# Optimization experiments

Hardware: AMD Instinct MI355X
Metric: run time of the kernel (lower is better)

Reference implementation:

```python
import jax, jax.numpy as jnp
import numpy as np

WINDOW = 47
PAD = WINDOW // 2


def _box_sum(x):
    """Separable 47x47 box-filter SUM with zero padding (NHWC).

    Mathematically identical to a full 2-D window sum but O(W) per pixel
    instead of O(W^2).
    """
    x = jax.lax.reduce_window(
        x, 0.0, jax.lax.add,
        window_dimensions=(1, WINDOW, 1, 1), window_strides=(1, 1, 1, 1),
        padding=[(0, 0), (PAD, PAD), (0, 0), (0, 0)])
    x = jax.lax.reduce_window(
        x, 0.0, jax.lax.add,
        window_dimensions=(1, 1, WINDOW, 1), window_strides=(1, 1, 1, 1),
        padding=[(0, 0), (0, 0), (PAD, PAD), (0, 0)])
    return x


def setup_inputs() -> dict:
    key = jax.random.key(0)
    targets = jax.random.normal(key, (128, 224, 224, 3), dtype=jnp.float32)
    return {"targets": targets}


def reference(targets) -> jnp.ndarray:
    B, H, W, C = targets.shape
    # Number of valid (non-pad) pixels per window position; shape [1,H,W,1].
    counts = _box_sum(jnp.ones((1, H, W, 1), dtype=targets.dtype))
    # Original module precomputes this as int32 via rint(avg_pool*W^2).
    targets_count = jnp.rint(counts).astype(jnp.int32)

    # avg_pool(count_include_pad=False) == windowed_sum / valid_count
    targets_mean = _box_sum(targets) / counts
    targets_square_mean = _box_sum(targets * targets) / counts

    targets_var = targets_square_mean - targets_mean * targets_mean
    # Bessel correction with edge-aware counts (int/int -> float true divide).
    targets_var = targets_var * (targets_count / (targets_count - 1))
    targets_var = jnp.maximum(targets_var, 0.0)

    return (targets - targets_mean) / jnp.sqrt(targets_var + 1e-06)
```

## Files before the change

kernel.cpp:

```cpp
#include <hip/hip_runtime.h>


namespace {
constexpr int H = 224;
constexpr int W = 224;
constexpr int C = 3;
constexpr int WC = W * C;
constexpr int RAD = 23;
constexpr int SB = 2;
constexpr int NSB = 7;
constexpr int TH = SB * NSB;
constexpr int PADW = 226;
constexpr int NROWS = SB * C;
}

__global__ __launch_bounds__(256, 8) void wnorm_kernel(
    const float* __restrict__ in, float* __restrict__ out) {
  __shared__ float2 vsq[NROWS][PADW];

  const int tid = threadIdx.x;
  const int lane = tid & 63;
  const int wv = tid >> 6;
  const int r0 = blockIdx.x * TH;
  const float* __restrict__ img = in + (size_t)blockIdx.y * (H * WC);
  float* __restrict__ oimg = out + (size_t)blockIdx.y * (H * WC);

  const bool own = (tid < W);
  const int w = tid;

  float S0 = 0.f, S1 = 0.f, S2 = 0.f, Q0 = 0.f, Q1 = 0.f, Q2 = 0.f;
  if (own) {
    const int rlo = r0 - RAD;
#pragma unroll 8
    for (int i = 0; i < 47; ++i) {
      const int r = rlo + i;
      const int rc = min(max(r, 0), H - 1);
      const float m = (r >= 0 && r < H) ? 1.f : 0.f;
      const float3 v = ((const float3*)(img + rc * WC))[w];
      const float x0 = v.x * m, x1 = v.y * m, x2 = v.z * m;
      S0 += x0; Q0 += x0 * x0;
      S1 += x1; Q1 += x1 * x1;
      S2 += x2; Q2 += x2 * x2;
    }
  }

  const int hiw = min(w + RAD, W - 1);
  const int low = w - RAD - 1;
  const float cww = (float)(hiw - max(w - RAD, 0) + 1);

  float xr0[SB], xr1[SB], xr2[SB];

  for (int sb = 0; sb < NSB; ++sb) {
    const int hb = r0 + sb * SB;

#pragma unroll
    for (int r = 0; r < SB; ++r) {
      const int h = hb + r;
      if (own) {
        vsq[r * C + 0][w] = make_float2(S0, Q0);
        vsq[r * C + 1][w] = make_float2(S1, Q1);
        vsq[r * C + 2][w] = make_float2(S2, Q2);
        const float3 xv = ((const float3*)(img + h * WC))[w];
        xr0[r] = xv.x; xr1[r] = xv.y; xr2[r] = xv.z;
      }
      const int ra = h + RAD + 1;
      const int rs = h - RAD;
      if (ra < H && own) {
        const float3 v = ((const float3*)(img + ra * WC))[w];
        S0 += v.x; Q0 += v.x * v.x;
        S1 += v.y; Q1 += v.y * v.y;
        S2 += v.z; Q2 += v.z * v.z;
      }
      if (rs >= 0 && own) {
        const float3 v = ((const float3*)(img + rs * WC))[w];
        S0 -= v.x; Q0 -= v.x * v.x;
        S1 -= v.y; Q1 -= v.y * v.y;
        S2 -= v.z; Q2 -= v.z * v.z;
      }
    }

    __syncthreads();

    for (int rr = wv; rr < NROWS; rr += 4) {
      const bool act = (lane < 56);
      const int w0 = lane << 2;
      float4* p4 = reinterpret_cast<float4*>(&vsq[rr][act ? w0 : 0]);
      float4 a = make_float4(0.f, 0.f, 0.f, 0.f), b = a;
      if (act) { a = p4[0]; b = p4[1]; }
      const float p0x = a.x,       p0y = a.y;
      const float p1x = p0x + a.z, p1y = p0y + a.w;
      const float p2x = p1x + b.x, p2y = p1y + b.y;
      const float p3x = p2x + b.z, p3y = p2y + b.w;
      float Tx = p3x, Ty = p3y;
#pragma unroll
      for (int d = 1; d < 64; d <<= 1) {
        const float sx = __shfl_up(Tx, d);
        const float sy = __shfl_up(Ty, d);
        if (lane >= d) { Tx += sx; Ty += sy; }
      }
      const float ex = Tx - p3x, ey = Ty - p3y;
      if (act) {
        p4[0] = make_float4(p0x + ex, p0y + ey, p1x + ex, p1y + ey);
        p4[1] = make_float4(p2x + ex, p2y + ey, p3x + ex, p3y + ey);
      }
    }

    __syncthreads();

    if (own) {
#pragma unroll
      for (int r = 0; r < SB; ++r) {
        const int h = hb + r;
        const float chh =
            (float)(min(h + RAD, H - 1) - max(h - RAD, 0) + 1);
        const float n = chh * cww;
        const float inv = __builtin_amdgcn_rcpf(n);
        const float i1 = __builtin_amdgcn_rcpf(n - 1.0f);
        const float xc[3] = {xr0[r], xr1[r], xr2[r]};
        float o[3];
#pragma unroll
        for (int c = 0; c < C; ++c) {
          const float2 Ph = vsq[r * C + c][hiw];
          const float2 Pl = (low >= 0) ? vsq[r * C + c][low]
                                       : make_float2(0.f, 0.f);
          const float HS = Ph.x - Pl.x;
          const float HQ = Ph.y - Pl.y;
          const float mean = HS * inv;
          float var = (HQ - HS * mean) * i1;
          var = fmaxf(var, 0.0f);
          o[c] = (xc[c] - mean) * rsqrtf(var + 1e-6f);
        }
        ((float3*)(oimg + h * WC))[w] = make_float3(o[0], o[1], o[2]);
      }
    }

    __syncthreads();
  }
}

extern "C" void kernel_launch(void* const* d_in, const int* in_sizes, int n_in,
                              void* d_out, int out_size, void* d_ws, size_t ws_size,
                              hipStream_t stream) {
  const float* in = (const float*)d_in[0];
  float* out = (float*)d_out;
  const int B = in_sizes[0] / (H * W * C);
  dim3 grid(H / TH, B);
  wnorm_kernel<<<grid, 256, 0, stream>>>(in, out);
}
```

Baseline: 185.2 us.

## Restructure to per-channel threads with taller row strips and XCD-aware block mapping

Each thread now owns a single (w,c) column element instead of three channels of a pixel, using 704 threads so loads are contiguous scalar floats rather than float3. Each block processes a 56-row quarter image in groups of 7 rows, which cuts the redundant 47-row vertical warm-up relative to the old 14-row strips. The grid is flattened and remapped so consecutive work items land on the same XCD, aiming for better L2 locality. Loads for a group of rows are batched up front to raise memory-level parallelism. The cost is fewer blocks in flight, larger shared memory per block, and more rows scanned per group between barriers.

```diff
diff --git a/kernel.cpp b/kernel.cpp
--- a/kernel.cpp
+++ b/kernel.cpp
@@ -7,40 +7,54 @@
 constexpr int C = 3;
 constexpr int WC = W * C;
 constexpr int RAD = 23;
-constexpr int SB = 2;
-constexpr int NSB = 7;
-constexpr int TH = SB * NSB;
+constexpr int QH = 56;
+constexpr int G = 7;
+constexpr int NG = QH / G;
+constexpr int NT = 704;
 constexpr int PADW = 226;
-constexpr int NROWS = SB * C;
 }
 
-__global__ __launch_bounds__(256, 8) void wnorm_kernel(
+__global__ __launch_bounds__(NT, 6) void wnorm_kernel(
     const float* __restrict__ in, float* __restrict__ out) {
-  __shared__ float2 vsq[NROWS][PADW];
+  __shared__ float2 vsq[G][C][PADW];
 
   const int tid = threadIdx.x;
   const int lane = tid & 63;
   const int wv = tid >> 6;
-  const int r0 = blockIdx.x * TH;
-  const float* __restrict__ img = in + (size_t)blockIdx.y * (H * WC);
-  float* __restrict__ oimg = out + (size_t)blockIdx.y * (H * WC);
 
-  const bool own = (tid < W);
-  const int w = tid;
+  const int nwg = gridDim.x;
+  const int chunk = nwg >> 3;
+  const int bid = blockIdx.x;
+  const int work = (bid & 7) * chunk + (bid >> 3);
+  const int img = work >> 2;
+  const int q = work & 3;
+  const int r0 = q * QH;
 
-  float S0 = 0.f, S1 = 0.f, S2 = 0.f, Q0 = 0.f, Q1 = 0.f, Q2 = 0.f;
+  const float* __restrict__ src = in + (size_t)img * (H * WC);
+  float* __restrict__ dst = out + (size_t)img * (H * WC);
+
+  const bool own = (tid < WC);
+  const int col = tid;
+  const int w = col / 3;
+  const int c = col - 3 * w;
+
+  float S = 0.f, Q = 0.f;
   if (own) {
-    const int rlo = r0 - RAD;
+    if (r0 == 0) {
 #pragma unroll 8
-    for (int i = 0; i < 47; ++i) {
-      const int r = rlo + i;
-      const int rc = min(max(r, 0), H - 1);
-      const float m = (r >= 0 && r < H) ? 1.f : 0.f;
-      const float3 v = ((const float3*)(img + rc * WC))[w];
-      const float x0 = v.x * m, x1 = v.y * m, x2 = v.z * m;
-      S0 += x0; Q0 += x0 * x0;
-      S1 += x1; Q1 += x1 * x1;
-      S2 += x2; Q2 += x2 * x2;
+      for (int i = 0; i < 47; ++i) {
+        const int r = i - RAD;
+        const int rc = max(r, 0);
+        const float m = (r >= 0) ? 1.f : 0.f;
+        const float x = src[rc * WC + col] * m;
+        S += x; Q += x * x;
+      }
+    } else {
+#pragma unroll 8
+      for (int i = 0; i < 47; ++i) {
+        const float x = src[(r0 - RAD + i) * WC + col];
+        S += x; Q += x * x;
+      }
     }
   }
 
@@ -48,43 +62,37 @@
   const int low = w - RAD - 1;
   const float cww = (float)(hiw - max(w - RAD, 0) + 1);
 
-  float xr0[SB], xr1[SB], xr2[SB];
+  for (int g = 0; g < NG; ++g) {
+    const int h0 = r0 + g * G;
 
-  for (int sb = 0; sb < NSB; ++sb) {
-    const int hb = r0 + sb * SB;
-
+    float xa[G], xs[G], xx[G];
+    if (own) {
 #pragma unroll
-    for (int r = 0; r < SB; ++r) {
-      const int h = hb + r;
-      if (own) {
-        vsq[r * C + 0][w] = make_float2(S0, Q0);
-        vsq[r * C + 1][w] = make_float2(S1, Q1);
-        vsq[r * C + 2][w] = make_float2(S2, Q2);
-        const float3 xv = ((const float3*)(img + h * WC))[w];
-        xr0[r] = xv.x; xr1[r] = xv.y; xr2[r] = xv.z;
+      for (int r = 0; r < G; ++r) {
+        const int h = h0 + r;
+        const int ra = h + RAD + 1;
+        const int rs = h - RAD;
+        const float ma = (ra < H) ? 1.f : 0.f;
+        const float ms = (rs >= 0) ? 1.f : 0.f;
+        xa[r] = src[min(ra, H - 1) * WC + col] * ma;
+        xs[r] = src[max(rs, 0) * WC + col] * ms;
+        xx[r] = src[h * WC + col];
       }
-      const int ra = h + RAD + 1;
-      const int rs = h - RAD;
-      if (ra < H && own) {
-        const float3 v = ((const float3*)(img + ra * WC))[w];
-        S0 += v.x; Q0 += v.x * v.x;
-        S1 += v.y; Q1 += v.y * v.y;
-        S2 += v.z; Q2 += v.z * v.z;
-      }
-      if (rs >= 0 && own) {
-        const float3 v = ((const float3*)(img + rs * WC))[w];
-        S0 -= v.x; Q0 -= v.x * v.x;
-        S1 -= v.y; Q1 -= v.y * v.y;
-        S2 -= v.z; Q2 -= v.z * v.z;
+#pragma unroll
+      for (int r = 0; r < G; ++r) {
+        vsq[r][c][w] = make_float2(S, Q);
+        S += xa[r]; Q += xa[r] * xa[r];
+        S -= xs[r]; Q -= xs[r] * xs[r];
       }
     }
 
     __syncthreads();
 
-    for (int rr = wv; rr < NROWS; rr += 4) {
+    for (int rr = wv; rr < G * C; rr += 11) {
+      const int sr = rr / 3, sc = rr - 3 * (rr / 3);
       const bool act = (lane < 56);
       const int w0 = lane << 2;
-      float4* p4 = reinterpret_cast<float4*>(&vsq[rr][act ? w0 : 0]);
+      float4* p4 = reinterpret_cast<float4*>(&vsq[sr][sc][act ? w0 : 0]);
       float4 a = make_float4(0.f, 0.f, 0.f, 0.f), b = a;
       if (act) { a = p4[0]; b = p4[1]; }
       const float p0x = a.x,       p0y = a.y;
@@ -109,28 +117,22 @@
 
     if (own) {
 #pragma unroll
-      for (int r = 0; r < SB; ++r) {
-        const int h = hb + r;
+      for (int r = 0; r < G; ++r) {
+        const int h = h0 + r;
         const float chh =
             (float)(min(h + RAD, H - 1) - max(h - RAD, 0) + 1);
         const float n = chh * cww;
         const float inv = __builtin_amdgcn_rcpf(n);
         const float i1 = __builtin_amdgcn_rcpf(n - 1.0f);
-        const float xc[3] = {xr0[r], xr1[r], xr2[r]};
-        float o[3];
-#pragma unroll
-        for (int c = 0; c < C; ++c) {
-          const float2 Ph = vsq[r * C + c][hiw];
-          const float2 Pl = (low >= 0) ? vsq[r * C + c][low]
-                                       : make_float2(0.f, 0.f);
-          const float HS = Ph.x - Pl.x;
-          const float HQ = Ph.y - Pl.y;
-          const float mean = HS * inv;
-          float var = (HQ - HS * mean) * i1;
-          var = fmaxf(var, 0.0f);
-          o[c] = (xc[c] - mean) * rsqrtf(var + 1e-6f);
-        }
-        ((float3*)(oimg + h * WC))[w] = make_float3(o[0], o[1], o[2]);
+        const float2 Ph = vsq[r][c][hiw];
+        const float2 Pl = (low >= 0) ? vsq[r][c][low]
+                                     : make_float2(0.f, 0.f);
+        const float HS = Ph.x - Pl.x;
+        const float HQ = Ph.y - Pl.y;
+        const float mean = HS * inv;
+        float var = (HQ - HS * mean) * i1;
+        var = fmaxf(var, 0.0f);
+        dst[h * WC + col] = (xx[r] - mean) * rsqrtf(var + 1e-6f);
       }
     }
 
@@ -144,6 +146,6 @@
   const float* in = (const float*)d_in[0];
   float* out = (float*)d_out;
   const int B = in_sizes[0] / (H * W * C);
-  dim3 grid(H / TH, B);
-  wnorm_kernel<<<grid, 256, 0, stream>>>(in, out);
+  const int nwg = B * 4;
+  wnorm_kernel<<<dim3(nwg), dim3(NT), 0, stream>>>(in, out);
 }
```

Result: faster. 166.2 us (-10.3%).
